# Optimization experiments

Measured on AMD Instinct MI355X. Metric: run time of the kernel, lower is better.

Reference implementation:

```python
import jax, jax.numpy as jnp
import numpy as np

B, L1, L2, H = 32, 512, 512, 768


def setup_inputs() -> dict:
    key = jax.random.key(0)
    k1, k2, k3, k4 = jax.random.split(key, 4)
    x = jax.random.normal(k1, (B, L1, H), dtype=jnp.float32)
    y = jax.random.normal(k2, (B, L2, H), dtype=jnp.float32)
    # y_mask: True = padding position to be masked out (torch masked_fill semantics)
    y_mask = jax.random.randint(k3, (B, L2), 0, 2).astype(bool)
    W = jax.random.normal(k4, (H, H), dtype=jnp.float32) * 0.02  # nn.Linear weight [out,in]
    b = jnp.zeros((H,), dtype=jnp.float32)
    return {"x": x, "y": y, "y_mask": y_mask, "W": W, "b": b}


def reference(x, y, y_mask, W, b):
    # Shared linear projection + ReLU on both sequences (nn.Linear: v @ W^T + b)
    x_proj = jax.nn.relu(jnp.einsum('bmh,oh->bmo', x, W) + b)
    y_proj = jax.nn.relu(jnp.einsum('bnh,oh->bno', y, W) + b)
    # Unscaled attention scores [B, L1, L2]
    scores = jnp.einsum('bmh,bnh->bmn', x_proj, y_proj)
    scores = jnp.where(y_mask[:, None, :], -jnp.inf, scores)
    alpha = jax.nn.softmax(scores, axis=-1)
    # Attention-weighted sum over the *original* y (not y_proj)
    matched_seq = jnp.einsum('bmn,bnh->bmh', alpha, y)
    return matched_seq
```

## Files before the change

### kernel.cpp

```cpp
#include <hip/hip_runtime.h>
#include <hip/hip_bf16.h>
#include <math.h>


typedef _Float16 f16x8 __attribute__((ext_vector_type(8)));
typedef float f32x4 __attribute__((ext_vector_type(4)));

__device__ __forceinline__ void gld_lds16(const void* g, void* l) {
  __builtin_amdgcn_global_load_lds(
      (const __attribute__((address_space(1))) unsigned*)g,
      (__attribute__((address_space(3))) unsigned*)l, 16, 0, 0);
}

__global__ __launch_bounds__(256) void cvt_f16_kernel(
    const float* __restrict__ src, _Float16* __restrict__ dst) {
  size_t i = ((size_t)blockIdx.x * 256 + threadIdx.x) * 8;
  float4 a = *(const float4*)&src[i];
  float4 b = *(const float4*)&src[i + 4];
  _Float16 h[8] = {(_Float16)a.x, (_Float16)a.y, (_Float16)a.z, (_Float16)a.w,
                   (_Float16)b.x, (_Float16)b.y, (_Float16)b.z, (_Float16)b.w};
  *(uint4*)&dst[i] = *(uint4*)h;
}

__global__ __launch_bounds__(256) void proj_mfma_kernel(
    const _Float16* __restrict__ A, const _Float16* __restrict__ W,
    const float* __restrict__ bias, _Float16* __restrict__ P) {
  const int K = 768, N = 768;
  __shared__ _Float16 As[128 * 32], Bs[128 * 32];
  int bm = blockIdx.x * 128, bn = blockIdx.y * 128;
  int tid = threadIdx.x, lane = tid & 63, wave = tid >> 6;
  int wm = (wave & 1) * 64, wn = (wave >> 1) * 64;
  int fr = lane & 15, fk = (lane >> 4) * 8;
  int lrow = lane >> 2, lcol = (lane & 3) << 3;

  f32x4 acc[4][4];
#pragma unroll
  for (int i = 0; i < 4; ++i)
#pragma unroll
    for (int j = 0; j < 4; ++j)
#pragma unroll
      for (int e = 0; e < 4; ++e) acc[i][j][e] = 0.f;

  for (int k0 = 0; k0 < K; k0 += 32) {
    __syncthreads();
#pragma unroll
    for (int t = 0; t < 2; ++t) {
      int row = wave * 32 + t * 16;
      gld_lds16(&A[(size_t)(bm + row + lrow) * K + k0 + lcol], &As[row * 32]);
      gld_lds16(&W[(size_t)(bn + row + lrow) * K + k0 + lcol], &Bs[row * 32]);
    }
    __syncthreads();
    f16x8 a[4], bb[4];
#pragma unroll
    for (int i = 0; i < 4; ++i) {
      a[i] = *(const f16x8*)&As[(wm + i * 16 + fr) * 32 + fk];
      bb[i] = *(const f16x8*)&Bs[(wn + i * 16 + fr) * 32 + fk];
    }
#pragma unroll
    for (int i = 0; i < 4; ++i)
#pragma unroll
      for (int j = 0; j < 4; ++j)
        acc[i][j] = __builtin_amdgcn_mfma_f32_16x16x32_f16(a[i], bb[j], acc[i][j], 0, 0, 0);
  }
#pragma unroll
  for (int i = 0; i < 4; ++i)
#pragma unroll
    for (int r = 0; r < 4; ++r) {
      int m = bm + wm + i * 16 + (lane >> 4) * 4 + r;
#pragma unroll
      for (int j = 0; j < 4; ++j) {
        int n = bn + wn + j * 16 + fr;
        P[(size_t)m * N + n] = (_Float16)fmaxf(acc[i][j][r] + bias[n], 0.f);
      }
    }
}

__global__ __launch_bounds__(256) void scores_mfma_kernel(
    const _Float16* __restrict__ Px, const _Float16* __restrict__ Py,
    const int* __restrict__ mask, float* __restrict__ S) {
  const int K = 768, L = 512;
  __shared__ _Float16 As[128 * 32], Bs[128 * 32];
  int b = blockIdx.z;
  size_t pb = (size_t)b * L * K;
  const int* mk = mask + (size_t)b * L;
  float* Sb = S + (size_t)b * L * L;
  int bm = blockIdx.x * 128, bn = blockIdx.y * 128;
  int tid = threadIdx.x, lane = tid & 63, wave = tid >> 6;
  int wm = (wave & 1) * 64, wn = (wave >> 1) * 64;
  int fr = lane & 15, fk = (lane >> 4) * 8;
  int lrow = lane >> 2, lcol = (lane & 3) << 3;

  f32x4 acc[4][4];
#pragma unroll
  for (int i = 0; i < 4; ++i)
#pragma unroll
    for (int j = 0; j < 4; ++j)
#pragma unroll
      for (int e = 0; e < 4; ++e) acc[i][j][e] = 0.f;

  for (int k0 = 0; k0 < K; k0 += 32) {
    __syncthreads();
#pragma unroll
    for (int t = 0; t < 2; ++t) {
      int row = wave * 32 + t * 16;
      gld_lds16(&Px[pb + (size_t)(bm + row + lrow) * K + k0 + lcol], &As[row * 32]);
      gld_lds16(&Py[pb + (size_t)(bn + row + lrow) * K + k0 + lcol], &Bs[row * 32]);
    }
    __syncthreads();
    f16x8 a[4], bb[4];
#pragma unroll
    for (int i = 0; i < 4; ++i) {
      a[i] = *(const f16x8*)&As[(wm + i * 16 + fr) * 32 + fk];
      bb[i] = *(const f16x8*)&Bs[(wn + i * 16 + fr) * 32 + fk];
    }
#pragma unroll
    for (int i = 0; i < 4; ++i)
#pragma unroll
      for (int j = 0; j < 4; ++j)
        acc[i][j] = __builtin_amdgcn_mfma_f32_16x16x32_f16(a[i], bb[j], acc[i][j], 0, 0, 0);
  }
#pragma unroll
  for (int i = 0; i < 4; ++i)
#pragma unroll
    for (int r = 0; r < 4; ++r) {
      int m = bm + wm + i * 16 + (lane >> 4) * 4 + r;
#pragma unroll
      for (int j = 0; j < 4; ++j) {
        int n = bn + wn + j * 16 + fr;
        Sb[(size_t)m * L + n] = mk[n] ? -INFINITY : acc[i][j][r];
      }
    }
}

__global__ __launch_bounds__(256) void softmax_kernel(
    const float* __restrict__ S, _Float16* __restrict__ Alpha) {
  size_t row = blockIdx.x;
  const float* p = S + row * 512;
  _Float16* q = Alpha + row * 512;
  int tid = threadIdx.x, lane = tid & 63, wid = tid >> 6;
  float2 v = *(const float2*)(p + tid * 2);

  float m = fmaxf(v.x, v.y);
#pragma unroll
  for (int off = 32; off > 0; off >>= 1) m = fmaxf(m, __shfl_down(m, off));
  __shared__ float redm[4], reds[4];
  if (lane == 0) redm[wid] = m;
  __syncthreads();
  m = fmaxf(fmaxf(redm[0], redm[1]), fmaxf(redm[2], redm[3]));

  float e0 = __expf(v.x - m);
  float e1 = __expf(v.y - m);
  float s = e0 + e1;
#pragma unroll
  for (int off = 32; off > 0; off >>= 1) s += __shfl_down(s, off);
  if (lane == 0) reds[wid] = s;
  __syncthreads();
  s = reds[0] + reds[1] + reds[2] + reds[3];
  float inv = 1.0f / s;
  q[tid * 2] = (_Float16)(e0 * inv);
  q[tid * 2 + 1] = (_Float16)(e1 * inv);
}

__global__ __launch_bounds__(256) void yT_kernel(const float* __restrict__ Y,
                                                 _Float16* __restrict__ YT) {
  __shared__ _Float16 T[64][65];
  int b = blockIdx.z;
  int n0 = blockIdx.x * 64, h0 = blockIdx.y * 64;
  const float* Yb = Y + (size_t)b * 512 * 768;
  _Float16* Tb = YT + (size_t)b * 768 * 512;
  int tid = threadIdx.x;
  int r = tid >> 4, c = (tid & 15) << 2;
#pragma unroll
  for (int i = 0; i < 4; ++i) {
    int rr = r + i * 16;
    float4 v = *(const float4*)&Yb[(size_t)(n0 + rr) * 768 + h0 + c];
    T[c + 0][rr] = (_Float16)v.x;
    T[c + 1][rr] = (_Float16)v.y;
    T[c + 2][rr] = (_Float16)v.z;
    T[c + 3][rr] = (_Float16)v.w;
  }
  __syncthreads();
  int hr = tid >> 2, nc = (tid & 3) << 4;
  _Float16* dst = &Tb[(size_t)(h0 + hr) * 512 + n0 + nc];
  _Float16 tmp[16];
#pragma unroll
  for (int j = 0; j < 16; ++j) tmp[j] = T[hr][nc + j];
  *(uint4*)&dst[0] = *(uint4*)&tmp[0];
  *(uint4*)&dst[8] = *(uint4*)&tmp[8];
}

__global__ __launch_bounds__(256) void attn_mfma_kernel(
    const _Float16* __restrict__ Alpha, const _Float16* __restrict__ YT,
    float* __restrict__ O) {
  const int L = 512, H = 768;
  __shared__ _Float16 As[128 * 32], Bs[128 * 32];
  int b = blockIdx.z;
  const _Float16* Ab = Alpha + (size_t)b * L * L;
  const _Float16* Yb = YT + (size_t)b * H * L;
  float* Ob = O + (size_t)b * L * H;
  int bm = blockIdx.x * 128, bn = blockIdx.y * 128;
  int tid = threadIdx.x, lane = tid & 63, wave = tid >> 6;
  int wm = (wave & 1) * 64, wn = (wave >> 1) * 64;
  int fr = lane & 15, fk = (lane >> 4) * 8;
  int lrow = lane >> 2, lcol = (lane & 3) << 3;

  f32x4 acc[4][4];
#pragma unroll
  for (int i = 0; i < 4; ++i)
#pragma unroll
    for (int j = 0; j < 4; ++j)
#pragma unroll
      for (int e = 0; e < 4; ++e) acc[i][j][e] = 0.f;

  for (int k0 = 0; k0 < L; k0 += 32) {
    __syncthreads();
#pragma unroll
    for (int t = 0; t < 2; ++t) {
      int row = wave * 32 + t * 16;
      gld_lds16(&Ab[(size_t)(bm + row + lrow) * L + k0 + lcol], &As[row * 32]);
      gld_lds16(&Yb[(size_t)(bn + row + lrow) * L + k0 + lcol], &Bs[row * 32]);
    }
    __syncthreads();
    f16x8 a[4], bb[4];
#pragma unroll
    for (int i = 0; i < 4; ++i) {
      a[i] = *(const f16x8*)&As[(wm + i * 16 + fr) * 32 + fk];
      bb[i] = *(const f16x8*)&Bs[(wn + i * 16 + fr) * 32 + fk];
    }
#pragma unroll
    for (int i = 0; i < 4; ++i)
#pragma unroll
      for (int j = 0; j < 4; ++j)
        acc[i][j] = __builtin_amdgcn_mfma_f32_16x16x32_f16(a[i], bb[j], acc[i][j], 0, 0, 0);
  }
#pragma unroll
  for (int i = 0; i < 4; ++i)
#pragma unroll
    for (int r = 0; r < 4; ++r) {
      int m = bm + wm + i * 16 + (lane >> 4) * 4 + r;
#pragma unroll
      for (int j = 0; j < 4; ++j) {
        int h = bn + wn + j * 16 + fr;
        Ob[(size_t)m * H + h] = acc[i][j][r];
      }
    }
}

extern "C" void kernel_launch(void* const* d_in, const int* in_sizes, int n_in,
                              void* d_out, int out_size, void* d_ws, size_t ws_size,
                              hipStream_t stream) {
  const float* x = (const float*)d_in[0];
  const float* y = (const float*)d_in[1];
  const int* y_mask = (const int*)d_in[2];
  const float* W = (const float*)d_in[3];
  const float* b = (const float*)d_in[4];
  float* out = (float*)d_out;

  const size_t E = (size_t)16384 * 768;
  _Float16* xh = (_Float16*)d_ws;
  _Float16* yh = xh + E;
  _Float16* Px = yh + E;
  _Float16* Py = Px + E;
  float* S = (float*)(Py + E);
  _Float16* Wh = (_Float16*)S;
  _Float16* alpha = xh;
  _Float16* yT = Px;

  dim3 blk(256);
  cvt_f16_kernel<<<dim3(6144), blk, 0, stream>>>(x, xh);
  cvt_f16_kernel<<<dim3(6144), blk, 0, stream>>>(y, yh);
  cvt_f16_kernel<<<dim3(288), blk, 0, stream>>>(W, Wh);
  proj_mfma_kernel<<<dim3(128, 6), blk, 0, stream>>>(xh, Wh, b, Px);
  proj_mfma_kernel<<<dim3(128, 6), blk, 0, stream>>>(yh, Wh, b, Py);
  scores_mfma_kernel<<<dim3(4, 4, 32), blk, 0, stream>>>(Px, Py, y_mask, S);
  yT_kernel<<<dim3(8, 12, 32), blk, 0, stream>>>(y, yT);
  softmax_kernel<<<dim3(32 * 512), blk, 0, stream>>>(S, alpha);
  attn_mfma_kernel<<<dim3(4, 6, 32), blk, 0, stream>>>(alpha, yT, out);
}
```

Measured before the change: 284.6 us.

## Fuse score GEMM with masked softmax and batch conversion/projection launches

The score GEMM now has each 512-thread block compute a full 64x512 row strip of scores. It then applies the mask and softmax in registers and writes fp16 alpha directly, so the fp32 score matrix round trip and the separate softmax kernel go away. The x/y conversion and the two projection launches are each merged into one launch via a grid dimension. The transpose now reads the already-converted fp16 y instead of fp32. The trade-off is a much smaller grid for the score step (256 blocks) with a larger shared-memory footprint, which may reduce occupancy and load balance.

```diff
diff --git a/kernel.cpp b/kernel.cpp
--- a/kernel.cpp
+++ b/kernel.cpp
@@ -10,6 +10,19 @@
   __builtin_amdgcn_global_load_lds(
       (const __attribute__((address_space(1))) unsigned*)g,
       (__attribute__((address_space(3))) unsigned*)l, 16, 0, 0);
+}
+
+__global__ __launch_bounds__(256) void cvt_xy_kernel(
+    const float* __restrict__ x, const float* __restrict__ y,
+    _Float16* __restrict__ xh, _Float16* __restrict__ yh) {
+  const float* src = blockIdx.y ? y : x;
+  _Float16* dst = blockIdx.y ? yh : xh;
+  size_t i = ((size_t)blockIdx.x * 256 + threadIdx.x) * 8;
+  float4 a = *(const float4*)&src[i];
+  float4 b = *(const float4*)&src[i + 4];
+  _Float16 h[8] = {(_Float16)a.x, (_Float16)a.y, (_Float16)a.z, (_Float16)a.w,
+                   (_Float16)b.x, (_Float16)b.y, (_Float16)b.z, (_Float16)b.w};
+  *(uint4*)&dst[i] = *(uint4*)h;
 }
 
 __global__ __launch_bounds__(256) void cvt_f16_kernel(
@@ -23,9 +36,12 @@
 }
 
 __global__ __launch_bounds__(256) void proj_mfma_kernel(
-    const _Float16* __restrict__ A, const _Float16* __restrict__ W,
-    const float* __restrict__ bias, _Float16* __restrict__ P) {
+    const _Float16* __restrict__ Xh, const _Float16* __restrict__ Yh,
+    const _Float16* __restrict__ W, const float* __restrict__ bias,
+    _Float16* __restrict__ Px, _Float16* __restrict__ Py) {
   const int K = 768, N = 768;
+  const _Float16* A = blockIdx.z ? Yh : Xh;
+  _Float16* P = blockIdx.z ? Py : Px;
   __shared__ _Float16 As[128 * 32], Bs[128 * 32];
   int bm = blockIdx.x * 128, bn = blockIdx.y * 128;
   int tid = threadIdx.x, lane = tid & 63, wave = tid >> 6;
@@ -75,18 +91,20 @@
     }
 }
 
-__global__ __launch_bounds__(256) void scores_mfma_kernel(
+__global__ __launch_bounds__(512) void scores_softmax_kernel(
     const _Float16* __restrict__ Px, const _Float16* __restrict__ Py,
-    const int* __restrict__ mask, float* __restrict__ S) {
+    const int* __restrict__ mask, _Float16* __restrict__ Alpha) {
   const int K = 768, L = 512;
-  __shared__ _Float16 As[128 * 32], Bs[128 * 32];
-  int b = blockIdx.z;
+  __shared__ _Float16 As[64 * 32];
+  __shared__ _Float16 Bs[512 * 32];
+  __shared__ float redm[8][64], reds[8][64];
+  int b = blockIdx.y;
   size_t pb = (size_t)b * L * K;
   const int* mk = mask + (size_t)b * L;
-  float* Sb = S + (size_t)b * L * L;
-  int bm = blockIdx.x * 128, bn = blockIdx.y * 128;
+  _Float16* Ab = Alpha + (size_t)b * L * L;
+  int bm = blockIdx.x * 64;
   int tid = threadIdx.x, lane = tid & 63, wave = tid >> 6;
-  int wm = (wave & 1) * 64, wn = (wave >> 1) * 64;
+  int wn = wave * 64;
   int fr = lane & 15, fk = (lane >> 4) * 8;
   int lrow = lane >> 2, lcol = (lane & 3) << 3;
 
@@ -101,16 +119,19 @@
   for (int k0 = 0; k0 < K; k0 += 32) {
     __syncthreads();
 #pragma unroll
-    for (int t = 0; t < 2; ++t) {
-      int row = wave * 32 + t * 16;
+    for (int t = 0; t < 4; ++t) {
+      int row = wave * 64 + t * 16;
+      gld_lds16(&Py[pb + (size_t)(row + lrow) * K + k0 + lcol], &Bs[row * 32]);
+    }
+    if (wave < 4) {
+      int row = wave * 16;
       gld_lds16(&Px[pb + (size_t)(bm + row + lrow) * K + k0 + lcol], &As[row * 32]);
-      gld_lds16(&Py[pb + (size_t)(bn + row + lrow) * K + k0 + lcol], &Bs[row * 32]);
     }
     __syncthreads();
     f16x8 a[4], bb[4];
 #pragma unroll
     for (int i = 0; i < 4; ++i) {
-      a[i] = *(const f16x8*)&As[(wm + i * 16 + fr) * 32 + fk];
+      a[i] = *(const f16x8*)&As[(i * 16 + fr) * 32 + fk];
       bb[i] = *(const f16x8*)&Bs[(wn + i * 16 + fr) * 32 + fk];
     }
 #pragma unroll
@@ -119,72 +140,102 @@
       for (int j = 0; j < 4; ++j)
         acc[i][j] = __builtin_amdgcn_mfma_f32_16x16x32_f16(a[i], bb[j], acc[i][j], 0, 0, 0);
   }
-#pragma unroll
-  for (int i = 0; i < 4; ++i)
-#pragma unroll
-    for (int r = 0; r < 4; ++r) {
-      int m = bm + wm + i * 16 + (lane >> 4) * 4 + r;
+
+  int mki[4];
+#pragma unroll
+  for (int j = 0; j < 4; ++j) mki[j] = mk[wn + j * 16 + fr];
+#pragma unroll
+  for (int i = 0; i < 4; ++i)
+#pragma unroll
+    for (int j = 0; j < 4; ++j)
+      if (mki[j]) {
+#pragma unroll
+        for (int r = 0; r < 4; ++r) acc[i][j][r] = -INFINITY;
+      }
+
+  int g4 = (lane >> 4) << 2;
+#pragma unroll
+  for (int i = 0; i < 4; ++i)
+#pragma unroll
+    for (int r = 0; r < 4; ++r) {
+      float m = fmaxf(fmaxf(acc[i][0][r], acc[i][1][r]),
+                      fmaxf(acc[i][2][r], acc[i][3][r]));
+      m = fmaxf(m, __shfl_xor(m, 1));
+      m = fmaxf(m, __shfl_xor(m, 2));
+      m = fmaxf(m, __shfl_xor(m, 4));
+      m = fmaxf(m, __shfl_xor(m, 8));
+      if (fr == 0) redm[wave][i * 16 + g4 + r] = m;
+    }
+  __syncthreads();
+  float M[4][4];
+#pragma unroll
+  for (int i = 0; i < 4; ++i)
+#pragma unroll
+    for (int r = 0; r < 4; ++r) {
+      int row = i * 16 + g4 + r;
+      float m = redm[0][row];
+#pragma unroll
+      for (int w = 1; w < 8; ++w) m = fmaxf(m, redm[w][row]);
+      M[i][r] = m;
+    }
+#pragma unroll
+  for (int i = 0; i < 4; ++i)
+#pragma unroll
+    for (int r = 0; r < 4; ++r) {
+      float s = 0.f;
 #pragma unroll
       for (int j = 0; j < 4; ++j) {
-        int n = bn + wn + j * 16 + fr;
-        Sb[(size_t)m * L + n] = mk[n] ? -INFINITY : acc[i][j][r];
+        float e = __expf(acc[i][j][r] - M[i][r]);
+        acc[i][j][r] = e;
+        s += e;
       }
-    }
-}
-
-__global__ __launch_bounds__(256) void softmax_kernel(
-    const float* __restrict__ S, _Float16* __restrict__ Alpha) {
-  size_t row = blockIdx.x;
-  const float* p = S + row * 512;
-  _Float16* q = Alpha + row * 512;
-  int tid = threadIdx.x, lane = tid & 63, wid = tid >> 6;
-  float2 v = *(const float2*)(p + tid * 2);
-
-  float m = fmaxf(v.x, v.y);
-#pragma unroll
-  for (int off = 32; off > 0; off >>= 1) m = fmaxf(m, __shfl_down(m, off));
-  __shared__ float redm[4], reds[4];
-  if (lane == 0) redm[wid] = m;
+      s += __shfl_xor(s, 1);
+      s += __shfl_xor(s, 2);
+      s += __shfl_xor(s, 4);
+      s += __shfl_xor(s, 8);
+      if (fr == 0) reds[wave][i * 16 + g4 + r] = s;
+    }
   __syncthreads();
-  m = fmaxf(fmaxf(redm[0], redm[1]), fmaxf(redm[2], redm[3]));
-
-  float e0 = __expf(v.x - m);
-  float e1 = __expf(v.y - m);
-  float s = e0 + e1;
-#pragma unroll
-  for (int off = 32; off > 0; off >>= 1) s += __shfl_down(s, off);
-  if (lane == 0) reds[wid] = s;
-  __syncthreads();
-  s = reds[0] + reds[1] + reds[2] + reds[3];
-  float inv = 1.0f / s;
-  q[tid * 2] = (_Float16)(e0 * inv);
-  q[tid * 2 + 1] = (_Float16)(e1 * inv);
-}
-
-__global__ __launch_bounds__(256) void yT_kernel(const float* __restrict__ Y,
-                                                 _Float16* __restrict__ YT) {
-  __shared__ _Float16 T[64][65];
+#pragma unroll
+  for (int i = 0; i < 4; ++i)
+#pragma unroll
+    for (int r = 0; r < 4; ++r) {
+      int row = i * 16 + g4 + r;
+      float s = reds[0][row];
+#pragma unroll
+      for (int w = 1; w < 8; ++w) s += reds[w][row];
+      float inv = 1.0f / s;
+#pragma unroll
+      for (int j = 0; j < 4; ++j)
+        Ab[(size_t)(bm + row) * L + wn + j * 16 + fr] =
+            (_Float16)(acc[i][j][r] * inv);
+    }
+}
+
+__global__ __launch_bounds__(256) void yT_kernel(
+    const _Float16* __restrict__ Yh, _Float16* __restrict__ YT) {
+  __shared__ unsigned short T[64][65];
   int b = blockIdx.z;
   int n0 = blockIdx.x * 64, h0 = blockIdx.y * 64;
-  const float* Yb = Y + (size_t)b * 512 * 768;
-  _Float16* Tb = YT + (size_t)b * 768 * 512;
+  const unsigned short* Yb = (const unsigned short*)Yh + (size_t)b * 512 * 768;
+  unsigned short* Tb = (unsigned short*)YT + (size_t)b * 768 * 512;
   int tid = threadIdx.x;
   int r = tid >> 4, c = (tid & 15) << 2;
 #pragma unroll
   for (int i = 0; i < 4; ++i) {
     int rr = r + i * 16;
-    float4 v = *(const float4*)&Yb[(size_t)(n0 + rr) * 768 + h0 + c];
-    T[c + 0][rr] = (_Float16)v.x;
-    T[c + 1][rr] = (_Float16)v.y;
-    T[c + 2][rr] = (_Float16)v.z;
-    T[c + 3][rr] = (_Float16)v.w;
+    ushort4 v = *(const ushort4*)&Yb[(size_t)(n0 + rr) * 768 + h0 + c];
+    T[c + 0][rr] = v.x;
+    T[c + 1][rr] = v.y;
+    T[c + 2][rr] = v.z;
+    T[c + 3][rr] = v.w;
   }
   __syncthreads();
   int hr = tid >> 2, nc = (tid & 3) << 4;
-  _Float16* dst = &Tb[(size_t)(h0 + hr) * 512 + n0 + nc];
-  _Float16 tmp[16];
+  unsigned short tmp[16];
 #pragma unroll
   for (int j = 0; j < 16; ++j) tmp[j] = T[hr][nc + j];
+  unsigned short* dst = &Tb[(size_t)(h0 + hr) * 512 + n0 + nc];
   *(uint4*)&dst[0] = *(uint4*)&tmp[0];
   *(uint4*)&dst[8] = *(uint4*)&tmp[8];
 }
@@ -261,19 +312,15 @@
   _Float16* yh = xh + E;
   _Float16* Px = yh + E;
   _Float16* Py = Px + E;
-  float* S = (float*)(Py + E);
-  _Float16* Wh = (_Float16*)S;
+  _Float16* Wh = Py + E;
   _Float16* alpha = xh;
   _Float16* yT = Px;
 
   dim3 blk(256);
-  cvt_f16_kernel<<<dim3(6144), blk, 0, stream>>>(x, xh);
-  cvt_f16_kernel<<<dim3(6144), blk, 0, stream>>>(y, yh);
+  cvt_xy_kernel<<<dim3(6144, 2), blk, 0, stream>>>(x, y, xh, yh);
   cvt_f16_kernel<<<dim3(288), blk, 0, stream>>>(W, Wh);
-  proj_mfma_kernel<<<dim3(128, 6), blk, 0, stream>>>(xh, Wh, b, Px);
-  proj_mfma_kernel<<<dim3(128, 6), blk, 0, stream>>>(yh, Wh, b, Py);
-  scores_mfma_kernel<<<dim3(4, 4, 32), blk, 0, stream>>>(Px, Py, y_mask, S);
-  yT_kernel<<<dim3(8, 12, 32), blk, 0, stream>>>(y, yT);
-  softmax_kernel<<<dim3(32 * 512), blk, 0, stream>>>(S, alpha);
+  proj_mfma_kernel<<<dim3(128, 6, 2), blk, 0, stream>>>(xh, yh, Wh, b, Px, Py);
+  scores_softmax_kernel<<<dim3(8, 32), dim3(512), 0, stream>>>(Px, Py, y_mask, alpha);
+  yT_kernel<<<dim3(8, 12, 32), blk, 0, stream>>>(yh, yT);
   attn_mfma_kernel<<<dim3(4, 6, 32), blk, 0, stream>>>(alpha, yT, out);
 }
```

Result: no change. 288.6 us (+1.4%).
